# Performance work log

Measured on AMD Instinct MI355X. Metric: run time of the kernel, lower is better.

The kernel has to match this reference:

```python
import jax, jax.numpy as jnp
import numpy as np


def _conv1x1(x, w, b):
    # 1x1 conv == per-pixel channel GEMM: w [Cout,Cin], x [B,C,H,W]
    return jnp.einsum('oi,bihw->bohw', w, x) + b[None, :, None, None]


def setup_inputs() -> dict:
    key = jax.random.key(0)
    ks = jax.random.split(key, 9)
    B, C, H, W = 8, 256, 128, 128
    s = 1.0 / np.sqrt(C)
    x = jax.random.normal(ks[0], (B, C, H, W), dtype=jnp.float32)
    wk = jax.random.normal(ks[1], (C, C), dtype=jnp.float32) * s
    bk = jax.random.normal(ks[2], (C,), dtype=jnp.float32) * 0.01
    wq = jax.random.normal(ks[3], (C, C), dtype=jnp.float32) * s
    bq = jax.random.normal(ks[4], (C,), dtype=jnp.float32) * 0.01
    wv = jax.random.normal(ks[5], (C, C), dtype=jnp.float32) * s
    bv = jax.random.normal(ks[6], (C,), dtype=jnp.float32) * 0.01
    wo = jax.random.normal(ks[7], (C, C), dtype=jnp.float32) * s
    bo = jax.random.normal(ks[8], (C,), dtype=jnp.float32) * 0.01
    return {'x': x, 'wk': wk, 'bk': bk, 'wq': wq, 'bq': bq,
            'wv': wv, 'bv': bv, 'wo': wo, 'bo': bo}


def reference(x, wk, bk, wq, bq, wv, bv, wo, bo):
    k = _conv1x1(x, wk, bk)   # [B,C,H,W]
    q = _conv1x1(x, wq, bq)
    v = _conv1x1(x, wv, bv)
    # transpose(key,-1,-2) @ query -> [B,C,W,W]
    scores = jnp.einsum('bchw,bchv->bcwv', k, q)
    # softmax over dim=0 (batch), as in the original module
    attn = jax.nn.softmax(scores, axis=0)
    # value @ attention_map -> [B,C,H,W]
    out = jnp.einsum('bchw,bcwv->bchv', v, attn)
    out = _conv1x1(out, wo, bo)
    return out + x
```

## Files before the change

### kernel.cpp

```cpp
#include <hip/hip_runtime.h>
#include <math.h>

#define B_ 8
#define C_ 256
#define H_ 128
#define W_ 128
#define HW_ (H_*W_)
#define PLANE ((size_t)C_*HW_)

typedef __attribute__((ext_vector_type(8))) short short8;
typedef __attribute__((ext_vector_type(4))) float f32x4;

static __device__ __forceinline__ unsigned short f2bf(float f) {
    unsigned u = __float_as_uint(f);
    u += 0x7FFF + ((u >> 16) & 1);
    return (unsigned short)(u >> 16);
}
static __device__ __forceinline__ float bf2f(unsigned short h) {
    return __uint_as_float(((unsigned)h) << 16);
}

#define SWZ(row, kbyte) ((((row) << 6) | (kbyte)) ^ (((row) & 7) << 4))

template<int NS, int MPS, bool RESID>
__global__ __launch_bounds__(256)
void conv_mfma(const float* __restrict__ X,
               const float* __restrict__ W0, const float* __restrict__ W1,
               const float* __restrict__ W2,
               const float* __restrict__ Bi0, const float* __restrict__ Bi1,
               const float* __restrict__ Bi2,
               const float* __restrict__ resid,
               float* __restrict__ Y0, float* __restrict__ Y1,
               float* __restrict__ Y2)
{
    constexpr int NROWS = NS * MPS;
    constexpr int MREP  = MPS / 16;
    constexpr int BN = 128, BK = 32;

    __shared__ unsigned short AhT[NROWS * BK], AlT[NROWS * BK];
    __shared__ unsigned short BhT[BN * BK],   BlT[BN * BK];
    __shared__ float biasLds[NROWS];

    const int b    = blockIdx.z;
    const int co0  = blockIdx.y * MPS;
    const int p0   = blockIdx.x * BN;
    const int t    = threadIdx.x;
    const int lane = t & 63;
    const int wv   = t >> 6;

    const float* Wp[3] = {W0, W1, W2};
    const float* Bp[3] = {Bi0, Bi1, Bi2};
    float*       Yp[3] = {Y0, Y1, Y2};
    const float* Xb = X + (size_t)b * PLANE;

    if (t < NROWS) {
        const int s = t / MPS, r = t % MPS;
        biasLds[t] = Bp[s][co0 + r];
    }

    f32x4 acc[NS][MREP][2];
#pragma unroll
    for (int s = 0; s < NS; ++s)
#pragma unroll
        for (int mr = 0; mr < MREP; ++mr)
#pragma unroll
            for (int nr = 0; nr < 2; ++nr)
                acc[s][mr][nr] = (f32x4){0.f, 0.f, 0.f, 0.f};

    const int kb = (lane >> 4) << 4;

    for (int k0 = 0; k0 < C_; k0 += BK) {
#pragma unroll
        for (int i = 0; i < NROWS / 32; ++i) {
            const int idx = t + (i << 8);
            const int row = idx >> 3;
            const int q4  = (idx & 7) << 2;
            const int s   = row / MPS;
            const int cl  = row % MPS;
            const float4 w4 = *(const float4*)(Wp[s] + (size_t)(co0 + cl) * C_ + (k0 + q4));
            const unsigned short h0 = f2bf(w4.x), h1 = f2bf(w4.y),
                                 h2 = f2bf(w4.z), h3 = f2bf(w4.w);
            const ushort4 hv = {h0, h1, h2, h3};
            const ushort4 lv = {f2bf(w4.x - bf2f(h0)), f2bf(w4.y - bf2f(h1)),
                                f2bf(w4.z - bf2f(h2)), f2bf(w4.w - bf2f(h3))};
            *(ushort4*)((char*)AhT + SWZ(row, q4 << 1)) = hv;
            *(ushort4*)((char*)AlT + SWZ(row, q4 << 1)) = lv;
        }
#pragma unroll
        for (int i = 0; i < 4; ++i) {
            const int ci = (i << 3) + (t & 7);
            const int p4 = (t >> 3) << 2;
            const float4 x4 = *(const float4*)(Xb + (size_t)(k0 + ci) * HW_ + (p0 + p4));
            const float xe[4] = {x4.x, x4.y, x4.z, x4.w};
#pragma unroll
            for (int e = 0; e < 4; ++e) {
                const unsigned short hh = f2bf(xe[e]);
                const unsigned short ll = f2bf(xe[e] - bf2f(hh));
                *(unsigned short*)((char*)BhT + SWZ(p4 + e, ci << 1)) = hh;
                *(unsigned short*)((char*)BlT + SWZ(p4 + e, ci << 1)) = ll;
            }
        }
        __syncthreads();

        short8 bfh[2], bfl[2];
        const int prow_base = (wv << 5) + (lane & 15);
#pragma unroll
        for (int nr = 0; nr < 2; ++nr) {
            const int prow = prow_base + (nr << 4);
            bfh[nr] = *(short8*)((char*)BhT + SWZ(prow, kb));
            bfl[nr] = *(short8*)((char*)BlT + SWZ(prow, kb));
        }
#pragma unroll
        for (int s = 0; s < NS; ++s) {
#pragma unroll
            for (int mr = 0; mr < MREP; ++mr) {
                const int arow = s * MPS + (mr << 4) + (lane & 15);
                const short8 afh = *(short8*)((char*)AhT + SWZ(arow, kb));
                const short8 afl = *(short8*)((char*)AlT + SWZ(arow, kb));
#pragma unroll
                for (int nr = 0; nr < 2; ++nr) {
                    acc[s][mr][nr] = __builtin_amdgcn_mfma_f32_16x16x32_bf16(
                        afh, bfh[nr], acc[s][mr][nr], 0, 0, 0);
                    acc[s][mr][nr] = __builtin_amdgcn_mfma_f32_16x16x32_bf16(
                        afh, bfl[nr], acc[s][mr][nr], 0, 0, 0);
                    acc[s][mr][nr] = __builtin_amdgcn_mfma_f32_16x16x32_bf16(
                        afl, bfh[nr], acc[s][mr][nr], 0, 0, 0);
                }
            }
        }
        __syncthreads();
    }

    const int r4   = (lane >> 4) << 2;
    const int pcol = p0 + (wv << 5) + (lane & 15);
#pragma unroll
    for (int s = 0; s < NS; ++s) {
        float* Y = Yp[s];
#pragma unroll
        for (int mr = 0; mr < MREP; ++mr) {
#pragma unroll
            for (int nr = 0; nr < 2; ++nr) {
                const f32x4 a = acc[s][mr][nr];
#pragma unroll
                for (int r = 0; r < 4; ++r) {
                    const int cl = (mr << 4) + r4 + r;
                    const int co = co0 + cl;
                    const size_t addr = (size_t)b * PLANE + (size_t)co * HW_
                                      + (size_t)(pcol + (nr << 4));
                    float val = a[r] + biasLds[s * MPS + cl];
                    if (RESID) val += resid[addr];
                    Y[addr] = val;
                }
            }
        }
    }
}

__global__ __launch_bounds__(256)
void scores_mfma(const float* __restrict__ Kt, float* __restrict__ Q)
{
    __shared__ unsigned short QTh[128 * 32], QTl[128 * 32];
    __shared__ unsigned short KTh[128 * 32], KTl[128 * 32];

    const int bc = blockIdx.x;
    const float* Kp = Kt + (size_t)bc * HW_;
    const float* Qp = Q  + (size_t)bc * HW_;
    const int t = threadIdx.x, lane = t & 63, wv = t >> 6;

    const int hhp = t & 15;
    const int vc  = (t >> 4) << 3;
    const int kb  = (lane >> 4) << 4;

    f32x4 acc[2][8];
#pragma unroll
    for (int mr = 0; mr < 2; ++mr)
#pragma unroll
        for (int nr = 0; nr < 8; ++nr)
            acc[mr][nr] = (f32x4){0.f, 0.f, 0.f, 0.f};

    for (int h0 = 0; h0 < H_; h0 += 32) {
        float qv[2][8], kv[2][8];
#pragma unroll
        for (int j = 0; j < 2; ++j) {
            const int hh = h0 + (hhp << 1) + j;
            const float4 q0 = *(const float4*)(Qp + (size_t)hh * W_ + vc);
            const float4 q1 = *(const float4*)(Qp + (size_t)hh * W_ + vc + 4);
            const float4 k0 = *(const float4*)(Kp + (size_t)hh * W_ + vc);
            const float4 k1 = *(const float4*)(Kp + (size_t)hh * W_ + vc + 4);
            qv[j][0]=q0.x; qv[j][1]=q0.y; qv[j][2]=q0.z; qv[j][3]=q0.w;
            qv[j][4]=q1.x; qv[j][5]=q1.y; qv[j][6]=q1.z; qv[j][7]=q1.w;
            kv[j][0]=k0.x; kv[j][1]=k0.y; kv[j][2]=k0.z; kv[j][3]=k0.w;
            kv[j][4]=k1.x; kv[j][5]=k1.y; kv[j][6]=k1.z; kv[j][7]=k1.w;
        }
#pragma unroll
        for (int e = 0; e < 8; ++e) {
            const int v = vc + e;
            const int off = SWZ(v, hhp << 2);
            const unsigned short qh0 = f2bf(qv[0][e]), qh1 = f2bf(qv[1][e]);
            const unsigned short kh0 = f2bf(kv[0][e]), kh1 = f2bf(kv[1][e]);
            *(ushort2*)((char*)QTh + off) = (ushort2){qh0, qh1};
            *(ushort2*)((char*)QTl + off) = (ushort2){f2bf(qv[0][e] - bf2f(qh0)),
                                                      f2bf(qv[1][e] - bf2f(qh1))};
            *(ushort2*)((char*)KTh + off) = (ushort2){kh0, kh1};
            *(ushort2*)((char*)KTl + off) = (ushort2){f2bf(kv[0][e] - bf2f(kh0)),
                                                      f2bf(kv[1][e] - bf2f(kh1))};
        }
        __syncthreads();

        short8 bh[8], bl[8];
#pragma unroll
        for (int nr = 0; nr < 8; ++nr) {
            const int wrow = (nr << 4) + (lane & 15);
            bh[nr] = *(short8*)((char*)KTh + SWZ(wrow, kb));
            bl[nr] = *(short8*)((char*)KTl + SWZ(wrow, kb));
        }
#pragma unroll
        for (int mr = 0; mr < 2; ++mr) {
            const int vrow = (wv << 5) + (mr << 4) + (lane & 15);
            const short8 ah = *(short8*)((char*)QTh + SWZ(vrow, kb));
            const short8 al = *(short8*)((char*)QTl + SWZ(vrow, kb));
#pragma unroll
            for (int nr = 0; nr < 8; ++nr) {
                acc[mr][nr] = __builtin_amdgcn_mfma_f32_16x16x32_bf16(ah, bh[nr], acc[mr][nr], 0, 0, 0);
                acc[mr][nr] = __builtin_amdgcn_mfma_f32_16x16x32_bf16(ah, bl[nr], acc[mr][nr], 0, 0, 0);
                acc[mr][nr] = __builtin_amdgcn_mfma_f32_16x16x32_bf16(al, bh[nr], acc[mr][nr], 0, 0, 0);
            }
        }
        __syncthreads();
    }

    float* Sp = Q + (size_t)bc * HW_;
    const int r4 = (lane >> 4) << 2;
#pragma unroll
    for (int mr = 0; mr < 2; ++mr) {
#pragma unroll
        for (int nr = 0; nr < 8; ++nr) {
            const f32x4 a = acc[mr][nr];
            const int w = (nr << 4) + (lane & 15);
#pragma unroll
            for (int r = 0; r < 4; ++r) {
                const int v = (wv << 5) + (mr << 4) + r4 + r;
                Sp[(size_t)v * W_ + w] = a[r];
            }
        }
    }
}

__global__ __launch_bounds__(256)
void softmax_pack(const float* __restrict__ S,
                  unsigned short* __restrict__ aH, unsigned short* __restrict__ aL)
{
    const size_t N = (size_t)C_ * HW_;
    const size_t idx = ((size_t)blockIdx.x * 256 + threadIdx.x) << 2;
    if (idx >= N) return;

    float4 vals[B_];
#pragma unroll
    for (int b = 0; b < B_; ++b) vals[b] = *(const float4*)(S + (size_t)b * N + idx);

    float4 mx = vals[0];
#pragma unroll
    for (int b = 1; b < B_; ++b) {
        mx.x = fmaxf(mx.x, vals[b].x); mx.y = fmaxf(mx.y, vals[b].y);
        mx.z = fmaxf(mx.z, vals[b].z); mx.w = fmaxf(mx.w, vals[b].w);
    }
    float4 sum = {0.f, 0.f, 0.f, 0.f};
#pragma unroll
    for (int b = 0; b < B_; ++b) {
        vals[b].x = expf(vals[b].x - mx.x); sum.x += vals[b].x;
        vals[b].y = expf(vals[b].y - mx.y); sum.y += vals[b].y;
        vals[b].z = expf(vals[b].z - mx.z); sum.z += vals[b].z;
        vals[b].w = expf(vals[b].w - mx.w); sum.w += vals[b].w;
    }
    const float4 inv = {1.f / sum.x, 1.f / sum.y, 1.f / sum.z, 1.f / sum.w};

    const int c = (int)(idx >> 14);
    const int r = (int)(idx & 16383);
    const int v = r >> 7, w = r & 127;
    const size_t tile_byte = ((size_t)(c << 2) + (w >> 5)) * 8192 + SWZ(v, (w & 31) << 1);

#pragma unroll
    for (int b = 0; b < B_; ++b) {
        const float o0 = vals[b].x * inv.x, o1 = vals[b].y * inv.y,
                    o2 = vals[b].z * inv.z, o3 = vals[b].w * inv.w;
        const unsigned short h0 = f2bf(o0), h1 = f2bf(o1),
                             h2 = f2bf(o2), h3 = f2bf(o3);
        char* bh = (char*)(aH + (size_t)b * N) + tile_byte;
        char* bl = (char*)(aL + (size_t)b * N) + tile_byte;
        *(ushort4*)bh = (ushort4){h0, h1, h2, h3};
        *(ushort4*)bl = (ushort4){f2bf(o0 - bf2f(h0)), f2bf(o1 - bf2f(h1)),
                                  f2bf(o2 - bf2f(h2)), f2bf(o3 - bf2f(h3))};
    }
}

__global__ __launch_bounds__(256)
void av_mfma(float* __restrict__ V,
             const unsigned short* __restrict__ aH,
             const unsigned short* __restrict__ aL)
{
    __shared__ unsigned short Vh[128 * 32], Vl[128 * 32];
    __shared__ unsigned short Ath[128 * 32], Atl[128 * 32];

    const int bc = blockIdx.x;
    float* Vp = V + (size_t)bc * HW_;
    const int t = threadIdx.x, lane = t & 63, wv = t >> 6;
    const int kb = (lane >> 4) << 4;

    const int hrow = t >> 1;
    const int wc   = (t & 1) << 4;

    f32x4 acc[2][8];
#pragma unroll
    for (int mr = 0; mr < 2; ++mr)
#pragma unroll
        for (int nr = 0; nr < 8; ++nr)
            acc[mr][nr] = (f32x4){0.f, 0.f, 0.f, 0.f};

    for (int ks = 0; ks < 4; ++ks) {
        const int w0 = ks << 5;
#pragma unroll
        for (int f = 0; f < 4; ++f) {
            const int wl = wc + (f << 2);
            const float4 v4 = *(const float4*)(Vp + (size_t)hrow * W_ + w0 + wl);
            const unsigned short h0 = f2bf(v4.x), h1 = f2bf(v4.y),
                                 h2 = f2bf(v4.z), h3 = f2bf(v4.w);
            const int off = SWZ(hrow, wl << 1);
            *(ushort4*)((char*)Vh + off) = (ushort4){h0, h1, h2, h3};
            *(ushort4*)((char*)Vl + off) = (ushort4){f2bf(v4.x - bf2f(h0)), f2bf(v4.y - bf2f(h1)),
                                                     f2bf(v4.z - bf2f(h2)), f2bf(v4.w - bf2f(h3))};
        }
        {
            const size_t tb = ((size_t)(bc << 2) + ks) << 12;
            const uint4* gh = (const uint4*)(aH + tb);
            const uint4* gl = (const uint4*)(aL + tb);
            ((uint4*)Ath)[t]       = gh[t];
            ((uint4*)Ath)[t + 256] = gh[t + 256];
            ((uint4*)Atl)[t]       = gl[t];
            ((uint4*)Atl)[t + 256] = gl[t + 256];
        }
        __syncthreads();

        short8 bh[8], bl[8];
#pragma unroll
        for (int nr = 0; nr < 8; ++nr) {
            const int vrow = (nr << 4) + (lane & 15);
            bh[nr] = *(short8*)((char*)Ath + SWZ(vrow, kb));
            bl[nr] = *(short8*)((char*)Atl + SWZ(vrow, kb));
        }
#pragma unroll
        for (int mr = 0; mr < 2; ++mr) {
            const int hr = (wv << 5) + (mr << 4) + (lane & 15);
            const short8 ah = *(short8*)((char*)Vh + SWZ(hr, kb));
            const short8 al = *(short8*)((char*)Vl + SWZ(hr, kb));
#pragma unroll
            for (int nr = 0; nr < 8; ++nr) {
                acc[mr][nr] = __builtin_amdgcn_mfma_f32_16x16x32_bf16(ah, bh[nr], acc[mr][nr], 0, 0, 0);
                acc[mr][nr] = __builtin_amdgcn_mfma_f32_16x16x32_bf16(ah, bl[nr], acc[mr][nr], 0, 0, 0);
                acc[mr][nr] = __builtin_amdgcn_mfma_f32_16x16x32_bf16(al, bh[nr], acc[mr][nr], 0, 0, 0);
            }
        }
        __syncthreads();
    }

    const int r4 = (lane >> 4) << 2;
#pragma unroll
    for (int mr = 0; mr < 2; ++mr) {
#pragma unroll
        for (int nr = 0; nr < 8; ++nr) {
            const f32x4 a = acc[mr][nr];
            const int vcol = (nr << 4) + (lane & 15);
#pragma unroll
            for (int r = 0; r < 4; ++r) {
                const int h = (wv << 5) + (mr << 4) + r4 + r;
                Vp[(size_t)h * W_ + vcol] = a[r];
            }
        }
    }
}

extern "C" void kernel_launch(void* const* d_in, const int* in_sizes, int n_in,
                              void* d_out, int out_size, void* d_ws, size_t ws_size,
                              hipStream_t stream)
{
    const float* x  = (const float*)d_in[0];
    const float* wk = (const float*)d_in[1];
    const float* bk = (const float*)d_in[2];
    const float* wq = (const float*)d_in[3];
    const float* bq = (const float*)d_in[4];
    const float* wv = (const float*)d_in[5];
    const float* bv = (const float*)d_in[6];
    const float* wo = (const float*)d_in[7];
    const float* bo = (const float*)d_in[8];
    float* out = (float*)d_out;

    const size_t NBUF = (size_t)B_ * PLANE;
    float* kbuf = (float*)d_ws;
    float* qbuf = kbuf + NBUF;
    float* vbuf = qbuf + NBUF;
    unsigned short* attnH = (unsigned short*)kbuf;
    unsigned short* attnL = attnH + NBUF;

    const dim3 gKQV(HW_ / 128, C_ / 32, B_);
    conv_mfma<3, 32, false><<<gKQV, 256, 0, stream>>>(
        x, wk, wq, wv, bk, bq, bv, nullptr, kbuf, qbuf, vbuf);

    scores_mfma<<<B_ * C_, 256, 0, stream>>>(kbuf, qbuf);
    softmax_pack<<<4096, 256, 0, stream>>>(qbuf, attnH, attnL);
    av_mfma<<<B_ * C_, 256, 0, stream>>>(vbuf, attnH, attnL);

    const dim3 gWO(HW_ / 128, C_ / 64, B_);
    conv_mfma<1, 64, true><<<gWO, 256, 0, stream>>>(
        vbuf, wo, nullptr, nullptr, bo, nullptr, nullptr, x, out, nullptr, nullptr);
}
```

Baseline: 870.4 us.

## Stage full-K input panel in LDS and stream weights directly from global

```diff
diff --git a/kernel.cpp b/kernel.cpp
--- a/kernel.cpp
+++ b/kernel.cpp
@@ -21,135 +21,126 @@
 }
 
 #define SWZ(row, kbyte) ((((row) << 6) | (kbyte)) ^ (((row) & 7) << 4))
-
-template<int NS, int MPS, bool RESID>
+#define PSWZ(row, kbyte) ((((row) << 9) | (kbyte)) ^ (((row) & 7) << 4))
+
+template<int NS, bool RESID>
 __global__ __launch_bounds__(256)
-void conv_mfma(const float* __restrict__ X,
-               const float* __restrict__ W0, const float* __restrict__ W1,
-               const float* __restrict__ W2,
-               const float* __restrict__ Bi0, const float* __restrict__ Bi1,
-               const float* __restrict__ Bi2,
-               const float* __restrict__ resid,
-               float* __restrict__ Y0, float* __restrict__ Y1,
-               float* __restrict__ Y2)
+void conv_panel(const float* __restrict__ X,
+                const float* __restrict__ W0, const float* __restrict__ W1,
+                const float* __restrict__ W2,
+                const float* __restrict__ Bi0, const float* __restrict__ Bi1,
+                const float* __restrict__ Bi2,
+                const float* __restrict__ resid,
+                float* __restrict__ Y0, float* __restrict__ Y1,
+                float* __restrict__ Y2)
 {
-    constexpr int NROWS = NS * MPS;
-    constexpr int MREP  = MPS / 16;
-    constexpr int BN = 128, BK = 32;
-
-    __shared__ unsigned short AhT[NROWS * BK], AlT[NROWS * BK];
-    __shared__ unsigned short BhT[BN * BK],   BlT[BN * BK];
-    __shared__ float biasLds[NROWS];
+    __shared__ unsigned short PH[32768], PL[32768];
+    __shared__ float biasL[NS * 256];
 
     const int b    = blockIdx.z;
-    const int co0  = blockIdx.y * MPS;
-    const int p0   = blockIdx.x * BN;
+    const int p0   = blockIdx.x << 7;
     const int t    = threadIdx.x;
     const int lane = t & 63;
     const int wv   = t >> 6;
+    const int l15  = lane & 15;
+    const int l4   = lane >> 4;
 
     const float* Wp[3] = {W0, W1, W2};
     const float* Bp[3] = {Bi0, Bi1, Bi2};
     float*       Yp[3] = {Y0, Y1, Y2};
     const float* Xb = X + (size_t)b * PLANE;
 
-    if (t < NROWS) {
-        const int s = t / MPS, r = t % MPS;
-        biasLds[t] = Bp[s][co0 + r];
-    }
-
-    f32x4 acc[NS][MREP][2];
-#pragma unroll
-    for (int s = 0; s < NS; ++s)
-#pragma unroll
-        for (int mr = 0; mr < MREP; ++mr)
-#pragma unroll
-            for (int nr = 0; nr < 2; ++nr)
-                acc[s][mr][nr] = (f32x4){0.f, 0.f, 0.f, 0.f};
-
-    const int kb = (lane >> 4) << 4;
-
-    for (int k0 = 0; k0 < C_; k0 += BK) {
-#pragma unroll
-        for (int i = 0; i < NROWS / 32; ++i) {
-            const int idx = t + (i << 8);
-            const int row = idx >> 3;
-            const int q4  = (idx & 7) << 2;
-            const int s   = row / MPS;
-            const int cl  = row % MPS;
-            const float4 w4 = *(const float4*)(Wp[s] + (size_t)(co0 + cl) * C_ + (k0 + q4));
-            const unsigned short h0 = f2bf(w4.x), h1 = f2bf(w4.y),
-                                 h2 = f2bf(w4.z), h3 = f2bf(w4.w);
-            const ushort4 hv = {h0, h1, h2, h3};
-            const ushort4 lv = {f2bf(w4.x - bf2f(h0)), f2bf(w4.y - bf2f(h1)),
-                                f2bf(w4.z - bf2f(h2)), f2bf(w4.w - bf2f(h3))};
-            *(ushort4*)((char*)AhT + SWZ(row, q4 << 1)) = hv;
-            *(ushort4*)((char*)AlT + SWZ(row, q4 << 1)) = lv;
-        }
-#pragma unroll
-        for (int i = 0; i < 4; ++i) {
-            const int ci = (i << 3) + (t & 7);
-            const int p4 = (t >> 3) << 2;
-            const float4 x4 = *(const float4*)(Xb + (size_t)(k0 + ci) * HW_ + (p0 + p4));
-            const float xe[4] = {x4.x, x4.y, x4.z, x4.w};
-#pragma unroll
-            for (int e = 0; e < 4; ++e) {
-                const unsigned short hh = f2bf(xe[e]);
-                const unsigned short ll = f2bf(xe[e] - bf2f(hh));
-                *(unsigned short*)((char*)BhT + SWZ(p4 + e, ci << 1)) = hh;
-                *(unsigned short*)((char*)BlT + SWZ(p4 + e, ci << 1)) = ll;
-            }
-        }
-        __syncthreads();
-
-        short8 bfh[2], bfl[2];
-        const int prow_base = (wv << 5) + (lane & 15);
-#pragma unroll
-        for (int nr = 0; nr < 2; ++nr) {
-            const int prow = prow_base + (nr << 4);
-            bfh[nr] = *(short8*)((char*)BhT + SWZ(prow, kb));
-            bfl[nr] = *(short8*)((char*)BlT + SWZ(prow, kb));
-        }
+#pragma unroll
+    for (int s = 0; s < NS; ++s) biasL[s * 256 + t] = Bp[s][t];
+
+#pragma unroll
+    for (int i = 0; i < 32; ++i) {
+        const int idx = t + (i << 8);
+        const int ci  = idx >> 5;
+        const int p4  = (idx & 31) << 2;
+        const float4 x4 = *(const float4*)(Xb + (size_t)ci * HW_ + (p0 + p4));
+        const float xe[4] = {x4.x, x4.y, x4.z, x4.w};
+#pragma unroll
+        for (int e = 0; e < 4; ++e) {
+            const unsigned short hh = f2bf(xe[e]);
+            const unsigned short ll = f2bf(xe[e] - bf2f(hh));
+            const int off = PSWZ(p4 + e, ci << 1);
+            *(unsigned short*)((char*)PH + off) = hh;
+            *(unsigned short*)((char*)PL + off) = ll;
+        }
+    }
+    __syncthreads();
+
+    const size_t ybase = (size_t)b * PLANE;
+    const int pcol = p0 + (wv << 5) + l15;
+
+    for (int coblk = 0; coblk < 8; ++coblk) {
+        f32x4 acc[NS][2][2];
+#pragma unroll
+        for (int s = 0; s < NS; ++s)
+#pragma unroll
+            for (int cr = 0; cr < 2; ++cr)
+#pragma unroll
+                for (int pr = 0; pr < 2; ++pr)
+                    acc[s][cr][pr] = (f32x4){0.f, 0.f, 0.f, 0.f};
+
+#pragma unroll 2
+        for (int ks = 0; ks < 8; ++ks) {
+            const int k0 = ks << 5;
+            short8 bh[2], bl[2];
+#pragma unroll
+            for (int pr = 0; pr < 2; ++pr) {
+                const int prow = (wv << 5) + (pr << 4) + l15;
+                const int off  = PSWZ(prow, (k0 + (l4 << 3)) << 1);
+                bh[pr] = *(short8*)((char*)PH + off);
+                bl[pr] = *(short8*)((char*)PL + off);
+            }
+#pragma unroll
+            for (int s = 0; s < NS; ++s) {
+#pragma unroll
+                for (int cr = 0; cr < 2; ++cr) {
+                    const int co = (coblk << 5) + (cr << 4) + l15;
+                    const float* wr = Wp[s] + (size_t)co * C_ + (k0 + (l4 << 3));
+                    const float4 wa = *(const float4*)wr;
+                    const float4 wb = *(const float4*)(wr + 4);
+                    const float wf[8] = {wa.x, wa.y, wa.z, wa.w,
+                                         wb.x, wb.y, wb.z, wb.w};
+                    short8 ah, al;
+#pragma unroll
+                    for (int j = 0; j < 8; ++j) {
+                        const unsigned short h = f2bf(wf[j]);
+                        ah[j] = (short)h;
+                        al[j] = (short)f2bf(wf[j] - bf2f(h));
+                    }
+#pragma unroll
+                    for (int pr = 0; pr < 2; ++pr) {
+                        acc[s][cr][pr] = __builtin_amdgcn_mfma_f32_16x16x32_bf16(
+                            ah, bh[pr], acc[s][cr][pr], 0, 0, 0);
+                        acc[s][cr][pr] = __builtin_amdgcn_mfma_f32_16x16x32_bf16(
+                            ah, bl[pr], acc[s][cr][pr], 0, 0, 0);
+                        acc[s][cr][pr] = __builtin_amdgcn_mfma_f32_16x16x32_bf16(
+                            al, bh[pr], acc[s][cr][pr], 0, 0, 0);
+                    }
+                }
+            }
+        }
+
 #pragma unroll
         for (int s = 0; s < NS; ++s) {
 #pragma unroll
-            for (int mr = 0; mr < MREP; ++mr) {
-                const int arow = s * MPS + (mr << 4) + (lane & 15);
-                const short8 afh = *(short8*)((char*)AhT + SWZ(arow, kb));
-                const short8 afl = *(short8*)((char*)AlT + SWZ(arow, kb));
-#pragma unroll
-                for (int nr = 0; nr < 2; ++nr) {
-                    acc[s][mr][nr] = __builtin_amdgcn_mfma_f32_16x16x32_bf16(
-                        afh, bfh[nr], acc[s][mr][nr], 0, 0, 0);
-                    acc[s][mr][nr] = __builtin_amdgcn_mfma_f32_16x16x32_bf16(
-                        afh, bfl[nr], acc[s][mr][nr], 0, 0, 0);
-                    acc[s][mr][nr] = __builtin_amdgcn_mfma_f32_16x16x32_bf16(
-                        afl, bfh[nr], acc[s][mr][nr], 0, 0, 0);
-                }
-            }
-        }
-        __syncthreads();
-    }
-
-    const int r4   = (lane >> 4) << 2;
-    const int pcol = p0 + (wv << 5) + (lane & 15);
-#pragma unroll
-    for (int s = 0; s < NS; ++s) {
-        float* Y = Yp[s];
-#pragma unroll
-        for (int mr = 0; mr < MREP; ++mr) {
-#pragma unroll
-            for (int nr = 0; nr < 2; ++nr) {
-                const f32x4 a = acc[s][mr][nr];
-#pragma unroll
-                for (int r = 0; r < 4; ++r) {
-                    const int cl = (mr << 4) + r4 + r;
-                    const int co = co0 + cl;
-                    const size_t addr = (size_t)b * PLANE + (size_t)co * HW_
-                                      + (size_t)(pcol + (nr << 4));
-                    float val = a[r] + biasLds[s * MPS + cl];
-                    if (RESID) val += resid[addr];
-                    Y[addr] = val;
+            for (int cr = 0; cr < 2; ++cr) {
+#pragma unroll
+                for (int pr = 0; pr < 2; ++pr) {
+                    const f32x4 a = acc[s][cr][pr];
+#pragma unroll
+                    for (int r = 0; r < 4; ++r) {
+                        const int co = (coblk << 5) + (cr << 4) + (l4 << 2) + r;
+                        const size_t addr = ybase + (size_t)co * HW_
+                                          + (size_t)(pcol + (pr << 4));
+                        float val = a[r] + biasL[s * 256 + co];
+                        if (RESID) val += resid[addr];
+                        Yp[s][addr] = val;
+                    }
                 }
             }
         }
@@ -400,15 +391,14 @@
     unsigned short* attnH = (unsigned short*)kbuf;
     unsigned short* attnL = attnH + NBUF;
 
-    const dim3 gKQV(HW_ / 128, C_ / 32, B_);
-    conv_mfma<3, 32, false><<<gKQV, 256, 0, stream>>>(
+    const dim3 gP(HW_ / 128, 1, B_);
+    conv_panel<3, false><<<gP, 256, 0, stream>>>(
         x, wk, wq, wv, bk, bq, bv, nullptr, kbuf, qbuf, vbuf);
 
     scores_mfma<<<B_ * C_, 256, 0, stream>>>(kbuf, qbuf);
     softmax_pack<<<4096, 256, 0, stream>>>(qbuf, attnH, attnL);
     av_mfma<<<B_ * C_, 256, 0, stream>>>(vbuf, attnH, attnL);
 
-    const dim3 gWO(HW_ / 128, C_ / 64, B_);
-    conv_mfma<1, 64, true><<<gWO, 256, 0, stream>>>(
+    conv_panel<1, true><<<gP, 256, 0, stream>>>(
         vbuf, wo, nullptr, nullptr, bo, nullptr, nullptr, x, out, nullptr, nullptr);
 }
```

Result: slower. 1.463 ms (+68.1%).
